# Kernel optimization log

Measured on AMD Instinct MI355X. Metric: run time of the kernel, lower is better.

## Reference

```python
import jax, jax.numpy as jnp
import numpy as np

N = 100000      # nodes
E = 1600000     # edges (before self-loops)
F_IN = 512      # input features
H = 8           # heads layer 1
D = 8           # per-head dim layer 1
C = 40          # classes (layer 2 out, heads=1)
NEG_SLOPE = 0.2 # PyG GATConv default negative_slope


def setup_inputs() -> dict:
    key = jax.random.key(0)
    ks = jax.random.split(key, 10)
    x = jax.random.normal(ks[0], (N, F_IN), jnp.float32)
    edge_index = jax.random.randint(ks[1], (2, E), 0, N, dtype=jnp.int32)
    W1 = jax.random.normal(ks[2], (F_IN, H * D), jnp.float32) / np.float32(np.sqrt(F_IN))
    att_src1 = jax.random.normal(ks[3], (H, D), jnp.float32) / np.float32(np.sqrt(D))
    att_dst1 = jax.random.normal(ks[4], (H, D), jnp.float32) / np.float32(np.sqrt(D))
    b1 = jnp.zeros((H * D,), jnp.float32)
    W2 = jax.random.normal(ks[5], (H * D, C), jnp.float32) / np.float32(np.sqrt(H * D))
    att_src2 = jax.random.normal(ks[6], (1, C), jnp.float32) / np.float32(np.sqrt(C))
    att_dst2 = jax.random.normal(ks[7], (1, C), jnp.float32) / np.float32(np.sqrt(C))
    b2 = jnp.zeros((C,), jnp.float32)
    return {"x": x, "edge_index": edge_index, "W1": W1, "att_src1": att_src1,
            "att_dst1": att_dst1, "b1": b1, "W2": W2, "att_src2": att_src2,
            "att_dst2": att_dst2, "b2": b2}


def _gat_layer(x, src, dst, W, a_src, a_dst, heads, dim):
    # Dense projection, then per-head attention logits.
    h = (x @ W).reshape(-1, heads, dim)            # [N, H, D]
    alpha_s = jnp.einsum('nhd,hd->nh', h, a_src)   # [N, H]
    alpha_d = jnp.einsum('nhd,hd->nh', h, a_dst)
    e = jax.nn.leaky_relu(alpha_s[src] + alpha_d[dst], NEG_SLOPE)  # [E, H]
    # Segment softmax over edges grouped by destination node.
    emax = jax.ops.segment_max(e, dst, num_segments=N)
    emax = jnp.where(jnp.isfinite(emax), emax, 0.0)
    ee = jnp.exp(e - emax[dst])
    denom = jax.ops.segment_sum(ee, dst, num_segments=N)
    alpha = ee / (denom[dst] + 1e-16)              # [E, H]
    # Scatter-aggregate weighted neighbor features.
    msg = h[src] * alpha[:, :, None]               # [E, H, D]
    return jax.ops.segment_sum(msg, dst, num_segments=N)  # [N, H, D]


def reference(x, edge_index, W1, att_src1, att_dst1, b1, W2, att_src2, att_dst2, b2):
    # PyG GATConv adds self-loops by default.
    loops = jnp.arange(N, dtype=edge_index.dtype)
    src = jnp.concatenate([edge_index[0], loops])
    dst = jnp.concatenate([edge_index[1], loops])
    # Layer 1: 8 heads, concat=True, then ELU. (dropouts identity in eval mode)
    h1 = _gat_layer(x, src, dst, W1, att_src1, att_dst1, H, D).reshape(N, H * D) + b1
    h1 = jax.nn.elu(h1)
    # Layer 2: 1 head, concat=False -> mean over heads (trivial for H=1).
    h2 = _gat_layer(h1, src, dst, W2, att_src2, att_dst2, 1, C)[:, 0, :] + b2
    return jax.nn.log_softmax(h2, axis=1)
```

## Files before the change

kernel.cpp:

```cpp
#include <hip/hip_runtime.h>

#define F_IN   512
#define HD     64
#define NHEAD  8
#define NC     40
#define NEG    0.2f

typedef __attribute__((ext_vector_type(8))) short bf16x8;
typedef __attribute__((ext_vector_type(4))) float f32x4;

__device__ __forceinline__ float lrelu(float x) { return x > 0.0f ? x : NEG * x; }

__device__ __forceinline__ short f2bf(float f) {
    unsigned u = __float_as_uint(f);
    u += 0x7FFF + ((u >> 16) & 1);
    return (short)(u >> 16);
}
__device__ __forceinline__ float bf2f(short h) {
    return __uint_as_float(((unsigned)(unsigned short)h) << 16);
}
__device__ __forceinline__ float bfl(unsigned u) { return __uint_as_float(u << 16); }
__device__ __forceinline__ float bfh(unsigned u) { return __uint_as_float(u & 0xFFFF0000u); }

__global__ void zero_kernel(int* __restrict__ p, int n) {
    int i = blockIdx.x * 256 + threadIdx.x;
    if (i < n) p[i] = 0;
}

__global__ __launch_bounds__(256) void scanA_kernel(const int* __restrict__ deg,
                                                    int* __restrict__ incl,
                                                    int* __restrict__ bsum, int Nn) {
    __shared__ int wsum[4];
    int t = threadIdx.x, b = blockIdx.x;
    int base = b * 1024 + t * 4;
    int v0 = (base + 0) < Nn ? deg[base + 0] : 0;
    int v1 = (base + 1) < Nn ? deg[base + 1] : 0;
    int v2 = (base + 2) < Nn ? deg[base + 2] : 0;
    int v3 = (base + 3) < Nn ? deg[base + 3] : 0;
    int p0 = v0, p1 = p0 + v1, p2 = p1 + v2, p3 = p2 + v3;
    int lane = t & 63, w = t >> 6;
    int sc = p3;
    for (int off = 1; off < 64; off <<= 1) {
        int u = __shfl_up(sc, off);
        if (lane >= off) sc += u;
    }
    if (lane == 63) wsum[w] = sc;
    __syncthreads();
    int woff = 0;
#pragma unroll
    for (int i = 0; i < 4; ++i) if (i < w) woff += wsum[i];
    int excl = woff + sc - p3;
    if (base + 0 < Nn) incl[base + 0] = excl + p0;
    if (base + 1 < Nn) incl[base + 1] = excl + p1;
    if (base + 2 < Nn) incl[base + 2] = excl + p2;
    if (base + 3 < Nn) incl[base + 3] = excl + p3;
    if (t == 0) bsum[b] = wsum[0] + wsum[1] + wsum[2] + wsum[3];
}

__global__ void scanB_kernel(int* __restrict__ bsum, int nb) {
    int lane = threadIdx.x;
    int a = lane < nb ? bsum[lane] : 0;
    int c = (lane + 64) < nb ? bsum[lane + 64] : 0;
    int sa = a, sc2 = c;
    for (int off = 1; off < 64; off <<= 1) {
        int u = __shfl_up(sa, off);  if (lane >= off) sa += u;
        int u2 = __shfl_up(sc2, off); if (lane >= off) sc2 += u2;
    }
    int totA = __shfl(sa, 63);
    int ea = sa - a;
    int ec = totA + sc2 - c;
    if (lane < nb) bsum[lane] = ea;
    if (lane + 64 < nb) bsum[lane + 64] = ec;
}

__global__ void scanC_kernel(const int* __restrict__ incl, const int* __restrict__ bsum,
                             int* __restrict__ rp, int Nn) {
    int i = blockIdx.x * 256 + threadIdx.x;
    if (i == 0) rp[0] = 0;
    if (i < Nn) rp[i + 1] = incl[i] + bsum[i >> 10];
}

__global__ void scatter_kernel(const int* __restrict__ src, const int* __restrict__ dst,
                               const int* __restrict__ pos, const int* __restrict__ rp,
                               int* __restrict__ col, int E) {
    int e = blockIdx.x * 256 + threadIdx.x;
    if (e < E) {
        int d = dst[e];
        col[rp[d] + pos[e]] = src[e];
    }
}

__global__ void wconv_kernel(const float* __restrict__ W, short* __restrict__ Whp) {
    int t = blockIdx.x * 256 + threadIdx.x;
    if (t >= F_IN * HD) return;
    int k = t >> 6, c = t & 63;
    Whp[((((k >> 3) * 64 + c)) << 3) + (k & 7)] = f2bf(W[t]);
}

#define G1_BM 64
__global__ __launch_bounds__(256) void g1c_kernel(const float* __restrict__ X,
                                                  const short* __restrict__ Whp,
                                                  const float* __restrict__ att_s,
                                                  const float* __restrict__ att_d,
                                                  unsigned short* __restrict__ Hp,
                                                  float* __restrict__ as1,
                                                  float* __restrict__ ad1,
                                                  const int* __restrict__ dst,
                                                  int* __restrict__ deg,
                                                  int* __restrict__ pos,
                                                  int Nn, int E, int nG1) {
    __shared__ short Bs[2][4096];
    int tid = threadIdx.x;

    if ((int)blockIdx.x >= nG1) {
        int e = ((int)blockIdx.x - nG1) * 256 + tid;
        if (e < E) pos[e] = atomicAdd(&deg[dst[e]], 1);
        return;
    }

    int wid = tid >> 6, lane = tid & 63;
    int lrow = lane & 15, kgrp = lane >> 4;
    int row0 = blockIdx.x * G1_BM;
    int rowA = row0 + wid * 16 + lrow;

    float ats[4], atd[4];
#pragma unroll
    for (int fc = 0; fc < 4; ++fc) { ats[fc] = att_s[fc * 16 + lrow]; atd[fc] = att_d[fc * 16 + lrow]; }

    f32x4 acc[4];
#pragma unroll
    for (int fc = 0; fc < 4; ++fc) acc[fc] = (f32x4){0.f, 0.f, 0.f, 0.f};

    bool valid = rowA < Nn;
    const float* xrow = X + (size_t)rowA * F_IN + kgrp * 8;
    const uint4* Wg = reinterpret_cast<const uint4*>(Whp);
    const float4 z4 = make_float4(0.f, 0.f, 0.f, 0.f);

    {
        uint4* Bv = reinterpret_cast<uint4*>(&Bs[0][0]);
        Bv[tid] = Wg[tid];
        Bv[tid + 256] = Wg[tid + 256];
    }
    float4 ac[2][2], an[2][2];
#pragma unroll
    for (int kb = 0; kb < 2; ++kb) {
        ac[kb][0] = valid ? *reinterpret_cast<const float4*>(xrow + kb * 32)     : z4;
        ac[kb][1] = valid ? *reinterpret_cast<const float4*>(xrow + kb * 32 + 4) : z4;
    }
    __syncthreads();

#pragma unroll
    for (int it = 0; it < F_IN / 64; ++it) {
        if (it + 1 < F_IN / 64) {
            uint4* Bv = reinterpret_cast<uint4*>(&Bs[(it + 1) & 1][0]);
            const uint4* Wt = Wg + (size_t)(it + 1) * 512;
            Bv[tid] = Wt[tid];
            Bv[tid + 256] = Wt[tid + 256];
#pragma unroll
            for (int kb = 0; kb < 2; ++kb) {
                const float* p = xrow + (it + 1) * 64 + kb * 32;
                an[kb][0] = valid ? *reinterpret_cast<const float4*>(p)     : z4;
                an[kb][1] = valid ? *reinterpret_cast<const float4*>(p + 4) : z4;
            }
        }
#pragma unroll
        for (int kb = 0; kb < 2; ++kb) {
            float fs[8] = {ac[kb][0].x, ac[kb][0].y, ac[kb][0].z, ac[kb][0].w,
                           ac[kb][1].x, ac[kb][1].y, ac[kb][1].z, ac[kb][1].w};
            bf16x8 af;
#pragma unroll
            for (int j = 0; j < 8; ++j) af[j] = f2bf(fs[j]);
#pragma unroll
            for (int fc = 0; fc < 4; ++fc) {
                bf16x8 b = *reinterpret_cast<const bf16x8*>(
                    &Bs[it & 1][(((kb * 4 + kgrp) * 64) + fc * 16 + lrow) * 8]);
                acc[fc] = __builtin_amdgcn_mfma_f32_16x16x32_bf16(af, b, acc[fc], 0, 0, 0);
            }
        }
        __syncthreads();
#pragma unroll
        for (int kb = 0; kb < 2; ++kb) {
            ac[kb][0] = an[kb][0];
            ac[kb][1] = an[kb][1];
        }
    }

#pragma unroll
    for (int r = 0; r < 4; ++r) {
        int gr = row0 + wid * 16 + kgrp * 4 + r;
        float hv[4], sp[4], dp[4];
#pragma unroll
        for (int fc = 0; fc < 4; ++fc) {
            hv[fc] = acc[fc][r];
            sp[fc] = hv[fc] * ats[fc];
            dp[fc] = hv[fc] * atd[fc];
        }
#pragma unroll
        for (int mask = 1; mask <= 4; mask <<= 1) {
#pragma unroll
            for (int fc = 0; fc < 4; ++fc) {
                sp[fc] += __shfl_xor(sp[fc], mask);
                dp[fc] += __shfl_xor(dp[fc], mask);
            }
        }
        if (gr < Nn) {
#pragma unroll
            for (int fc = 0; fc < 4; ++fc)
                Hp[(size_t)gr * HD + fc * 16 + lrow] = (unsigned short)f2bf(hv[fc]);
            if ((lane & 7) == 0) {
                int hh = lrow >> 3;
#pragma unroll
                for (int fc = 0; fc < 4; ++fc) {
                    as1[gr * NHEAD + fc * 2 + hh] = sp[fc];
                    ad1[gr * NHEAD + fc * 2 + hh] = dp[fc];
                }
            }
        }
    }
}

__global__ __launch_bounds__(256) void agg1_kernel(const unsigned short* __restrict__ Hp,
                                                   const float* __restrict__ as1,
                                                   const float* __restrict__ ad1,
                                                   const int* __restrict__ col,
                                                   const int* __restrict__ rp,
                                                   const float* __restrict__ b1,
                                                   float* __restrict__ h1, int Nn) {
    int n = blockIdx.x * 4 + (threadIdx.x >> 6);
    int lane = threadIdx.x & 63;
    if (n >= Nn) return;
    int slot = lane >> 3, j = lane & 7;
    int beg = rp[n], end = rp[n + 1];
    float adv1 = ad1[n * NHEAD + j];
    float acc[8] = {0, 0, 0, 0, 0, 0, 0, 0};
    float dw = 0.f;
    for (int t = beg + slot; t < end; t += 8) {
        int s = col[t];
        float w = __expf(lrelu(as1[s * NHEAD + j] + adv1));
        dw += w;
        uint4 u = *reinterpret_cast<const uint4*>(&Hp[(size_t)s * HD + j * 8]);
        acc[0] += w * bfl(u.x); acc[1] += w * bfh(u.x);
        acc[2] += w * bfl(u.y); acc[3] += w * bfh(u.y);
        acc[4] += w * bfl(u.z); acc[5] += w * bfh(u.z);
        acc[6] += w * bfl(u.w); acc[7] += w * bfh(u.w);
    }
#pragma unroll
    for (int mask = 8; mask < 64; mask <<= 1) {
#pragma unroll
        for (int i = 0; i < 8; ++i) acc[i] += __shfl_xor(acc[i], mask);
        dw += __shfl_xor(dw, mask);
    }
    float w = __expf(lrelu(as1[n * NHEAD + j] + adv1));
    uint4 u = *reinterpret_cast<const uint4*>(&Hp[(size_t)n * HD + j * 8]);
    acc[0] += w * bfl(u.x); acc[1] += w * bfh(u.x);
    acc[2] += w * bfl(u.y); acc[3] += w * bfh(u.y);
    acc[4] += w * bfl(u.z); acc[5] += w * bfh(u.z);
    acc[6] += w * bfl(u.w); acc[7] += w * bfh(u.w);
    dw += w;
    float invd = 1.0f / (dw + 1e-16f);
    float4 b0 = *reinterpret_cast<const float4*>(&b1[j * 8]);
    float4 b4 = *reinterpret_cast<const float4*>(&b1[j * 8 + 4]);
    float bb[8] = {b0.x, b0.y, b0.z, b0.w, b4.x, b4.y, b4.z, b4.w};
#pragma unroll
    for (int i = 0; i < 8; ++i) {
        float v = acc[i] * invd + bb[i];
        acc[i] = v > 0.0f ? v : __expf(v) - 1.0f;
    }
    if (slot == 0) {
        float4 o0 = make_float4(acc[0], acc[1], acc[2], acc[3]);
        float4 o1 = make_float4(acc[4], acc[5], acc[6], acc[7]);
        *reinterpret_cast<float4*>(&h1[(size_t)n * HD + j * 8]) = o0;
        *reinterpret_cast<float4*>(&h1[(size_t)n * HD + j * 8 + 4]) = o1;
    }
}

#define G2R 64
__global__ __launch_bounds__(256) void gemm2_kernel(const float* __restrict__ H1,
                                                    const float* __restrict__ W2,
                                                    const float* __restrict__ asw,
                                                    const float* __restrict__ adw,
                                                    unsigned int* __restrict__ h2p,
                                                    float* __restrict__ as2,
                                                    float* __restrict__ ad2, int Nn) {
    __shared__ float Hs[G2R][HD + 1];
    __shared__ float W2s[HD][NC];
    __shared__ float asv[NC], adv[NC];
    int tid = threadIdx.x;
    for (int i = tid; i < HD * NC; i += 256) W2s[i / NC][i % NC] = W2[i];
    if (tid < NC) { asv[tid] = asw[tid]; adv[tid] = adw[tid]; }
    int row0 = blockIdx.x * G2R;
#pragma unroll
    for (int i = 0; i < 4; ++i) {
        int linear = i * 1024 + tid * 4;
        int r = linear >> 6, c = linear & 63;
        int gr = row0 + r;
        float4 v = make_float4(0.f, 0.f, 0.f, 0.f);
        if (gr < Nn) v = *reinterpret_cast<const float4*>(&H1[(size_t)gr * HD + c]);
        Hs[r][c + 0] = v.x; Hs[r][c + 1] = v.y; Hs[r][c + 2] = v.z; Hs[r][c + 3] = v.w;
    }
    __syncthreads();
    int row = tid >> 2, cg = tid & 3;
    int gr = row0 + row;
    float acc[10];
#pragma unroll
    for (int jj = 0; jj < 10; ++jj) acc[jj] = 0.0f;
    for (int k = 0; k < HD; ++k) {
        float a = Hs[row][k];
#pragma unroll
        for (int jj = 0; jj < 10; ++jj) acc[jj] += a * W2s[k][cg * 10 + jj];
    }
    float sa = 0.0f, da = 0.0f;
#pragma unroll
    for (int jj = 0; jj < 10; ++jj) {
        sa += acc[jj] * asv[cg * 10 + jj];
        da += acc[jj] * adv[cg * 10 + jj];
    }
    sa += __shfl_xor(sa, 1); sa += __shfl_xor(sa, 2);
    da += __shfl_xor(da, 1); da += __shfl_xor(da, 2);
    if (gr < Nn) {
        if (cg == 0) { as2[gr] = sa; ad2[gr] = da; }
#pragma unroll
        for (int jj = 0; jj < 5; ++jj) {
            unsigned int u = ((unsigned int)(unsigned short)f2bf(acc[2 * jj + 1]) << 16) |
                             (unsigned short)f2bf(acc[2 * jj]);
            h2p[(size_t)gr * 20 + cg * 5 + jj] = u;
        }
    }
}

__global__ __launch_bounds__(256) void agg2_kernel(const unsigned int* __restrict__ h2p,
                                                   const float* __restrict__ as2,
                                                   const float* __restrict__ ad2,
                                                   const int* __restrict__ col,
                                                   const int* __restrict__ rp,
                                                   const float* __restrict__ b2,
                                                   float* __restrict__ out, int Nn) {
    int n = blockIdx.x * 4 + (threadIdx.x >> 6);
    int lane = threadIdx.x & 63;
    if (n >= Nn) return;
    int slot = lane >> 4, l16 = lane & 15;
    bool act = l16 < 10;
    int beg = rp[n], end = rp[n + 1];
    float adv = ad2[n];
    float4 acc = make_float4(0.f, 0.f, 0.f, 0.f);
    float dw = 0.f;
    for (int t = beg + slot; t < end; t += 4) {
        int s = col[t];
        float w = __expf(lrelu(as2[s] + adv));
        dw += w;
        if (act) {
            uint2 u = *reinterpret_cast<const uint2*>(&h2p[(size_t)s * 20 + l16 * 2]);
            acc.x += w * bfl(u.x); acc.y += w * bfh(u.x);
            acc.z += w * bfl(u.y); acc.w += w * bfh(u.y);
        }
    }
#pragma unroll
    for (int mask = 16; mask < 64; mask <<= 1) {
        acc.x += __shfl_xor(acc.x, mask);
        acc.y += __shfl_xor(acc.y, mask);
        acc.z += __shfl_xor(acc.z, mask);
        acc.w += __shfl_xor(acc.w, mask);
        dw    += __shfl_xor(dw, mask);
    }
    float w = __expf(lrelu(as2[n] + adv));
    dw += w;
    float invd = 1.0f / (dw + 1e-16f);
    if (act) {
        uint2 u = *reinterpret_cast<const uint2*>(&h2p[(size_t)n * 20 + l16 * 2]);
        float4 bb = *reinterpret_cast<const float4*>(&b2[l16 * 4]);
        acc.x = (acc.x + w * bfl(u.x)) * invd + bb.x;
        acc.y = (acc.y + w * bfh(u.x)) * invd + bb.y;
        acc.z = (acc.z + w * bfl(u.y)) * invd + bb.z;
        acc.w = (acc.w + w * bfh(u.y)) * invd + bb.w;
    }
    float mloc = act ? fmaxf(fmaxf(acc.x, acc.y), fmaxf(acc.z, acc.w)) : -INFINITY;
#pragma unroll
    for (int mask = 1; mask < 16; mask <<= 1) mloc = fmaxf(mloc, __shfl_xor(mloc, mask));
    float s4 = act ? (__expf(acc.x - mloc) + __expf(acc.y - mloc) +
                      __expf(acc.z - mloc) + __expf(acc.w - mloc)) : 0.0f;
#pragma unroll
    for (int mask = 1; mask < 16; mask <<= 1) s4 += __shfl_xor(s4, mask);
    float lse = mloc + __logf(s4);
    if (slot == 0 && act) {
        float4 o = make_float4(acc.x - lse, acc.y - lse, acc.z - lse, acc.w - lse);
        *reinterpret_cast<float4*>(&out[(size_t)n * NC + l16 * 4]) = o;
    }
}

extern "C" void kernel_launch(void* const* d_in, const int* in_sizes, int n_in,
                              void* d_out, int out_size, void* d_ws, size_t ws_size,
                              hipStream_t stream) {
    const float* x    = (const float*)d_in[0];
    const int*   ei   = (const int*)d_in[1];
    const float* W1   = (const float*)d_in[2];
    const float* as1w = (const float*)d_in[3];
    const float* ad1w = (const float*)d_in[4];
    const float* b1   = (const float*)d_in[5];
    const float* W2   = (const float*)d_in[6];
    const float* as2w = (const float*)d_in[7];
    const float* ad2w = (const float*)d_in[8];
    const float* b2   = (const float*)d_in[9];
    float* out = (float*)d_out;

    int Nn = in_sizes[0] / F_IN;
    int E  = in_sizes[1] / 2;
    const int* srcv = ei;
    const int* dstv = ei + E;

    char* ws = (char*)d_ws;
    size_t off = 0;
    auto alloc = [&](size_t bytes) { size_t cur = off; off += (bytes + 255) & ~255ULL; return cur; };
    unsigned short* Hp = (unsigned short*)(ws + alloc((size_t)Nn * HD * 2));
    float* h1   = (float*)(ws + alloc((size_t)Nn * HD * 4));
    float* as1v = (float*)(ws + alloc((size_t)Nn * NHEAD * 4));
    float* ad1v = (float*)(ws + alloc((size_t)Nn * NHEAD * 4));
    unsigned int* h2p = (unsigned int*)(ws + alloc((size_t)Nn * 20 * 4));
    float* as2v = (float*)(ws + alloc((size_t)Nn * 4));
    float* ad2v = (float*)(ws + alloc((size_t)Nn * 4));
    int* deg  = (int*)(ws + alloc((size_t)Nn * 4));
    int* incl = (int*)(ws + alloc((size_t)Nn * 4));
    int* rp   = (int*)(ws + alloc((size_t)(Nn + 1) * 4));
    int* pos  = (int*)(ws + alloc((size_t)E * 4));
    int* col  = (int*)(ws + alloc((size_t)E * 4));
    int* bsum = (int*)(ws + alloc(256 * 4));
    short* Whp = (short*)(ws + alloc((size_t)F_IN * HD * 2));

    int nb   = (Nn + 1023) / 1024;
    int nG1  = (Nn + G1_BM - 1) / G1_BM;
    int nCNT = (E + 255) / 256;

    zero_kernel<<<(Nn + 255) / 256, 256, 0, stream>>>(deg, Nn);
    wconv_kernel<<<(F_IN * HD + 255) / 256, 256, 0, stream>>>(W1, Whp);
    g1c_kernel<<<nG1 + nCNT, 256, 0, stream>>>(x, Whp, as1w, ad1w, Hp, as1v, ad1v,
                                               dstv, deg, pos, Nn, E, nG1);
    scanA_kernel<<<nb, 256, 0, stream>>>(deg, incl, bsum, Nn);
    scanB_kernel<<<1, 64, 0, stream>>>(bsum, nb);
    scanC_kernel<<<(Nn + 255) / 256, 256, 0, stream>>>(incl, bsum, rp, Nn);
    scatter_kernel<<<(E + 255) / 256, 256, 0, stream>>>(srcv, dstv, pos, rp, col, E);

    agg1_kernel<<<(Nn + 3) / 4, 256, 0, stream>>>(Hp, as1v, ad1v, col, rp, b1, h1, Nn);
    gemm2_kernel<<<(Nn + G2R - 1) / G2R, 256, 0, stream>>>(h1, W2, as2w, ad2w, h2p, as2v, ad2v, Nn);
    agg2_kernel<<<(Nn + 3) / 4, 256, 0, stream>>>(h2p, as2v, ad2v, col, rp, b2, out, Nn);
}
```

Baseline: 366.3 us.

## Privatize degree counters into eight partitions and restage GEMM weight loads

Result: no change. 367.9 us (+0.4%).

```diff
diff --git a/kernel.cpp b/kernel.cpp
--- a/kernel.cpp
+++ b/kernel.cpp
@@ -27,17 +27,23 @@
     if (i < n) p[i] = 0;
 }
 
-__global__ __launch_bounds__(256) void scanA_kernel(const int* __restrict__ deg,
+__global__ __launch_bounds__(256) void scanA_kernel(const int* __restrict__ deg8,
                                                     int* __restrict__ incl,
                                                     int* __restrict__ bsum, int Nn) {
     __shared__ int wsum[4];
     int t = threadIdx.x, b = blockIdx.x;
     int base = b * 1024 + t * 4;
-    int v0 = (base + 0) < Nn ? deg[base + 0] : 0;
-    int v1 = (base + 1) < Nn ? deg[base + 1] : 0;
-    int v2 = (base + 2) < Nn ? deg[base + 2] : 0;
-    int v3 = (base + 3) < Nn ? deg[base + 3] : 0;
-    int p0 = v0, p1 = p0 + v1, p2 = p1 + v2, p3 = p2 + v3;
+    int v[4] = {0, 0, 0, 0};
+#pragma unroll
+    for (int j = 0; j < 4; ++j) {
+        if (base + j < Nn) {
+            int s = 0;
+#pragma unroll
+            for (int p = 0; p < 8; ++p) s += deg8[(size_t)p * Nn + base + j];
+            v[j] = s;
+        }
+    }
+    int p0 = v[0], p1 = p0 + v[1], p2 = p1 + v[2], p3 = p2 + v[3];
     int lane = t & 63, w = t >> 6;
     int sc = p3;
     for (int off = 1; off < 64; off <<= 1) {
@@ -74,19 +80,30 @@
 }
 
 __global__ void scanC_kernel(const int* __restrict__ incl, const int* __restrict__ bsum,
-                             int* __restrict__ rp, int Nn) {
+                             const int* __restrict__ deg8, int* __restrict__ rp,
+                             int* __restrict__ rpo, int Nn) {
     int i = blockIdx.x * 256 + threadIdx.x;
     if (i == 0) rp[0] = 0;
-    if (i < Nn) rp[i + 1] = incl[i] + bsum[i >> 10];
+    if (i < Nn) {
+        int c[8], total = 0;
+#pragma unroll
+        for (int p = 0; p < 8; ++p) { c[p] = deg8[(size_t)p * Nn + i]; total += c[p]; }
+        int v = incl[i] + bsum[i >> 10];
+        rp[i + 1] = v;
+        int run = v - total;
+#pragma unroll
+        for (int p = 0; p < 8; ++p) { rpo[(size_t)p * Nn + i] = run; run += c[p]; }
+    }
 }
 
 __global__ void scatter_kernel(const int* __restrict__ src, const int* __restrict__ dst,
-                               const int* __restrict__ pos, const int* __restrict__ rp,
-                               int* __restrict__ col, int E) {
+                               const int* __restrict__ pos, const int* __restrict__ rpo,
+                               int* __restrict__ col, int E, int Nn, int nG1) {
     int e = blockIdx.x * 256 + threadIdx.x;
     if (e < E) {
         int d = dst[e];
-        col[rp[d] + pos[e]] = src[e];
+        int p = (nG1 + (e >> 8)) & 7;
+        col[rpo[(size_t)p * Nn + d] + pos[e]] = src[e];
     }
 }
 
@@ -106,7 +123,7 @@
                                                   float* __restrict__ as1,
                                                   float* __restrict__ ad1,
                                                   const int* __restrict__ dst,
-                                                  int* __restrict__ deg,
+                                                  int* __restrict__ deg8,
                                                   int* __restrict__ pos,
                                                   int Nn, int E, int nG1) {
     __shared__ short Bs[2][4096];
@@ -114,7 +131,8 @@
 
     if ((int)blockIdx.x >= nG1) {
         int e = ((int)blockIdx.x - nG1) * 256 + tid;
-        if (e < E) pos[e] = atomicAdd(&deg[dst[e]], 1);
+        int p = blockIdx.x & 7;
+        if (e < E) pos[e] = atomicAdd(&deg8[(size_t)p * Nn + dst[e]], 1);
         return;
     }
 
@@ -136,26 +154,26 @@
     const uint4* Wg = reinterpret_cast<const uint4*>(Whp);
     const float4 z4 = make_float4(0.f, 0.f, 0.f, 0.f);
 
-    {
-        uint4* Bv = reinterpret_cast<uint4*>(&Bs[0][0]);
-        Bv[tid] = Wg[tid];
-        Bv[tid + 256] = Wg[tid + 256];
-    }
+    uint4 w0 = Wg[tid], w1 = Wg[tid + 256];
     float4 ac[2][2], an[2][2];
 #pragma unroll
     for (int kb = 0; kb < 2; ++kb) {
         ac[kb][0] = valid ? *reinterpret_cast<const float4*>(xrow + kb * 32)     : z4;
         ac[kb][1] = valid ? *reinterpret_cast<const float4*>(xrow + kb * 32 + 4) : z4;
     }
+    {
+        uint4* Bv = reinterpret_cast<uint4*>(&Bs[0][0]);
+        Bv[tid] = w0;
+        Bv[tid + 256] = w1;
+    }
     __syncthreads();
 
 #pragma unroll
     for (int it = 0; it < F_IN / 64; ++it) {
-        if (it + 1 < F_IN / 64) {
-            uint4* Bv = reinterpret_cast<uint4*>(&Bs[(it + 1) & 1][0]);
-            const uint4* Wt = Wg + (size_t)(it + 1) * 512;
-            Bv[tid] = Wt[tid];
-            Bv[tid + 256] = Wt[tid + 256];
+        bool more = (it + 1) < F_IN / 64;
+        if (more) {
+            w0 = Wg[(size_t)(it + 1) * 512 + tid];
+            w1 = Wg[(size_t)(it + 1) * 512 + tid + 256];
 #pragma unroll
             for (int kb = 0; kb < 2; ++kb) {
                 const float* p = xrow + (it + 1) * 64 + kb * 32;
@@ -177,12 +195,17 @@
                 acc[fc] = __builtin_amdgcn_mfma_f32_16x16x32_bf16(af, b, acc[fc], 0, 0, 0);
             }
         }
+        if (more) {
+            uint4* Bn = reinterpret_cast<uint4*>(&Bs[(it + 1) & 1][0]);
+            Bn[tid] = w0;
+            Bn[tid + 256] = w1;
+#pragma unroll
+            for (int kb = 0; kb < 2; ++kb) {
+                ac[kb][0] = an[kb][0];
+                ac[kb][1] = an[kb][1];
+            }
+        }
         __syncthreads();
-#pragma unroll
-        for (int kb = 0; kb < 2; ++kb) {
-            ac[kb][0] = an[kb][0];
-            ac[kb][1] = an[kb][1];
-        }
     }
 
 #pragma unroll
@@ -417,9 +440,10 @@
     unsigned int* h2p = (unsigned int*)(ws + alloc((size_t)Nn * 20 * 4));
     float* as2v = (float*)(ws + alloc((size_t)Nn * 4));
     float* ad2v = (float*)(ws + alloc((size_t)Nn * 4));
-    int* deg  = (int*)(ws + alloc((size_t)Nn * 4));
+    int* deg8 = (int*)(ws + alloc((size_t)8 * Nn * 4));
     int* incl = (int*)(ws + alloc((size_t)Nn * 4));
     int* rp   = (int*)(ws + alloc((size_t)(Nn + 1) * 4));
+    int* rpo  = (int*)(ws + alloc((size_t)8 * Nn * 4));
     int* pos  = (int*)(ws + alloc((size_t)E * 4));
     int* col  = (int*)(ws + alloc((size_t)E * 4));
     int* bsum = (int*)(ws + alloc(256 * 4));
@@ -429,14 +453,14 @@
     int nG1  = (Nn + G1_BM - 1) / G1_BM;
     int nCNT = (E + 255) / 256;
 
-    zero_kernel<<<(Nn + 255) / 256, 256, 0, stream>>>(deg, Nn);
+    zero_kernel<<<(8 * Nn + 255) / 256, 256, 0, stream>>>(deg8, 8 * Nn);
     wconv_kernel<<<(F_IN * HD + 255) / 256, 256, 0, stream>>>(W1, Whp);
     g1c_kernel<<<nG1 + nCNT, 256, 0, stream>>>(x, Whp, as1w, ad1w, Hp, as1v, ad1v,
-                                               dstv, deg, pos, Nn, E, nG1);
-    scanA_kernel<<<nb, 256, 0, stream>>>(deg, incl, bsum, Nn);
+                                               dstv, deg8, pos, Nn, E, nG1);
+    scanA_kernel<<<nb, 256, 0, stream>>>(deg8, incl, bsum, Nn);
     scanB_kernel<<<1, 64, 0, stream>>>(bsum, nb);
-    scanC_kernel<<<(Nn + 255) / 256, 256, 0, stream>>>(incl, bsum, rp, Nn);
-    scatter_kernel<<<(E + 255) / 256, 256, 0, stream>>>(srcv, dstv, pos, rp, col, E);
+    scanC_kernel<<<(Nn + 255) / 256, 256, 0, stream>>>(incl, bsum, deg8, rp, rpo, Nn);
+    scatter_kernel<<<(E + 255) / 256, 256, 0, stream>>>(srcv, dstv, pos, rpo, col, E, Nn, nG1);
 
     agg1_kernel<<<(Nn + 3) / 4, 256, 0, stream>>>(Hp, as1v, ad1v, col, rp, b1, h1, Nn);
     gemm2_kernel<<<(Nn + G2R - 1) / G2R, 256, 0, stream>>>(h1, W2, as2w, ad2w, h2p, as2v, ad2v, Nn);
```
